# Optimization experiments

Hardware: AMD Instinct MI355X
Metric: run time of the kernel (lower is better)

Reference implementation:

```python
import jax, jax.numpy as jnp
import numpy as np

# dims
B_, L_, DIN, H, DOUT, NL = 2, 1024, 512, 768, 512, 4
ED, N, K = H, 16, 4            # expand_factor=1 -> d_inner=H; d_state=16; d_conv=4
DTR = (H + 15) // 16           # dt_rank = ceil(d_model/16) = 48


def setup_inputs() -> dict:
    key = jax.random.key(0)
    ks = iter(jax.random.split(key, 32))
    def g(shape, s=0.02):
        return jax.random.normal(next(ks), shape, jnp.float32) * s
    inp = dict(
        x=jax.random.normal(next(ks), (B_, L_, DIN), jnp.float32),
        in_proj_w=g((H, DIN)), in_proj_b=jnp.zeros((H,), jnp.float32),
        out_proj_w=g((DOUT, H)), out_proj_b=jnp.zeros((DOUT,), jnp.float32),
        ln1_w=jnp.ones((NL, H), jnp.float32), ln1_b=jnp.zeros((NL, H), jnp.float32),
        ln2_w=jnp.ones((NL, H), jnp.float32), ln2_b=jnp.zeros((NL, H), jnp.float32),
        ffn_w1=g((NL, 4 * H, H)), ffn_b1=jnp.zeros((NL, 4 * H), jnp.float32),
        ffn_w2=g((NL, H, 4 * H)), ffn_b2=jnp.zeros((NL, H), jnp.float32),
        rms_w=jnp.ones((NL, ED), jnp.float32),
        m_in_w=g((NL, 2 * ED, H)),
        conv_w=g((NL, ED, 1, K), 0.2), conv_b=jnp.zeros((NL, ED), jnp.float32),
        xproj_w=g((NL, DTR + 2 * N, ED)),
        dt_w=g((NL, ED, DTR), 0.1), dt_b=g((NL, ED), 0.1),
        A_log=jnp.log(jnp.tile(jnp.arange(1, N + 1, dtype=jnp.float32), (NL, ED, 1))),
        Dp=jnp.ones((NL, ED), jnp.float32),
        m_out_w=g((NL, H, ED)),
    )
    return inp


def _layernorm(x, w, b):
    m = x.mean(-1, keepdims=True)
    v = ((x - m) ** 2).mean(-1, keepdims=True)
    return (x - m) / jnp.sqrt(v + 1e-5) * w + b


def _rmsnorm(x, w):
    return x * jax.lax.rsqrt((x * x).mean(-1, keepdims=True) + 1e-5) * w


def _selective_scan(dA, dBx):
    # h_t = dA_t * h_{t-1} + dBx_t, done as a parallel associative scan over L
    def comb(c1, c2):
        a1, b1 = c1
        a2, b2 = c2
        return a1 * a2, a2 * b1 + b2
    _, h = jax.lax.associative_scan(comb, (dA, dBx), axis=1)
    return h  # (B, L, ED, N)


def _mamba(x, rw, iw, cw, cb, xw, dw, db, Alog, Dp, ow):
    # mambapy ResidualBlock: x + MambaBlock(RMSNorm(x))
    xn = _rmsnorm(x, rw)
    xz = xn @ iw.T                             # (B, L, 2*ED)
    xi, z = jnp.split(xz, 2, axis=-1)
    # causal depthwise conv1d (padding = K-1 left)
    xc = jax.lax.conv_general_dilated(
        xi.transpose(0, 2, 1), cw, (1,), [(K - 1, 0)],
        feature_group_count=ED, dimension_numbers=('NCH', 'OIH', 'NCH'))
    xi = jax.nn.silu(xc.transpose(0, 2, 1) + cb)
    dbc = xi @ xw.T                            # (B, L, DTR + 2N)
    d = dbc[..., :DTR]
    Bm = dbc[..., DTR:DTR + N]
    Cm = dbc[..., DTR + N:]
    delta = jax.nn.softplus(d @ dw.T + db)     # (B, L, ED)
    A = -jnp.exp(Alog)                         # (ED, N)
    dA = jnp.exp(delta[..., None] * A)         # (B, L, ED, N)
    dBx = (delta * xi)[..., None] * Bm[:, :, None, :]
    h = _selective_scan(dA, dBx)
    y = jnp.einsum('blen,bln->ble', h, Cm) + Dp * xi
    y = y * jax.nn.silu(z)
    return x + y @ ow.T


def reference(x, in_proj_w, in_proj_b, out_proj_w, out_proj_b,
              ln1_w, ln1_b, ln2_w, ln2_b,
              ffn_w1, ffn_b1, ffn_w2, ffn_b2,
              rms_w, m_in_w, conv_w, conv_b, xproj_w,
              dt_w, dt_b, A_log, Dp, m_out_w):
    h = x @ in_proj_w.T + in_proj_b
    for i in range(NL):
        h = h + _mamba(_layernorm(h, ln1_w[i], ln1_b[i]),
                       rms_w[i], m_in_w[i], conv_w[i], conv_b[i], xproj_w[i],
                       dt_w[i], dt_b[i], A_log[i], Dp[i], m_out_w[i])
        hn = _layernorm(h, ln2_w[i], ln2_b[i])
        h = h + jax.nn.relu(hn @ ffn_w1[i].T + ffn_b1[i]) @ ffn_w2[i].T + ffn_b2[i]
    return h @ out_proj_w.T + out_proj_b
```

## Files before the change

### kernel.cpp

```cpp
#include <hip/hip_runtime.h>
#include <stdint.h>

typedef unsigned short u16;
typedef __attribute__((ext_vector_type(8))) short short8;
typedef __attribute__((ext_vector_type(4))) float f32x4;

static __device__ __forceinline__ u16 f2bf(float f){
  unsigned int x = __float_as_uint(f);
  unsigned int r = (x + 0x7FFFu + ((x >> 16) & 1u)) >> 16;
  return (u16)r;
}
static __device__ __forceinline__ float bf2f(u16 u){
  return __uint_as_float(((unsigned int)u) << 16);
}

__global__ __launch_bounds__(256) void cvt_f32_bf16(const float* __restrict__ in,
                                                    u16* __restrict__ out, int n){
  int i = (blockIdx.x * 256 + threadIdx.x) * 4;
  int stride = gridDim.x * 256 * 4;
  for (; i < n; i += stride){
    float4 v = *reinterpret_cast<const float4*>(in + i);
    union { u16 u[4]; unsigned long long ll; } o;
    o.u[0] = f2bf(v.x); o.u[1] = f2bf(v.y); o.u[2] = f2bf(v.z); o.u[3] = f2bf(v.w);
    *reinterpret_cast<unsigned long long*>(out + i) = o.ll;
  }
}

__global__ __launch_bounds__(256) void build_dbc(const float* __restrict__ dt_w,
                                                 const float* __restrict__ xproj_w,
                                                 u16* __restrict__ out){
  const int total = 4 * 896 * 768;
  for (int idx = blockIdx.x * 256 + threadIdx.x; idx < total; idx += gridDim.x * 256){
    int l = idx / (896 * 768);
    int rem = idx - l * 896 * 768;
    int row = rem / 768;
    int k = rem - row * 768;
    float v = 0.f;
    if (row < 768){
      const float* dtr = dt_w + ((size_t)l * 768 + row) * 48;
      const float* xp  = xproj_w + (size_t)l * 80 * 768 + k;
      #pragma unroll 8
      for (int j = 0; j < 48; j++) v += dtr[j] * xp[(size_t)j * 768];
    } else if (row < 800){
      v = xproj_w[(size_t)l * 80 * 768 + (size_t)(48 + row - 768) * 768 + k];
    }
    out[idx] = f2bf(v);
  }
}

__global__ __launch_bounds__(256) void ln_rms_kernel(const float* __restrict__ in,
                                                     const float* __restrict__ w,
                                                     const float* __restrict__ b,
                                                     const float* __restrict__ rw,
                                                     float* __restrict__ xln,
                                                     u16* __restrict__ outB){
  int row = blockIdx.x;
  const float* x = in + (size_t)row * 768;
  int t = threadIdx.x;
  float v0 = x[t], v1 = x[t + 256], v2 = x[t + 512];
  float s = v0 + v1 + v2;
  float s2 = v0 * v0 + v1 * v1 + v2 * v2;
  #pragma unroll
  for (int off = 1; off < 64; off <<= 1){ s += __shfl_xor(s, off); s2 += __shfl_xor(s2, off); }
  __shared__ float red[8];
  int wid = t >> 6, lane = t & 63;
  if (lane == 0){ red[wid] = s; red[4 + wid] = s2; }
  __syncthreads();
  s = red[0] + red[1] + red[2] + red[3];
  s2 = red[4] + red[5] + red[6] + red[7];
  float mean = s * (1.f / 768.f);
  float var = s2 * (1.f / 768.f) - mean * mean;
  float rstd = rsqrtf(var + 1e-5f);
  float o0 = (v0 - mean) * rstd * w[t] + b[t];
  float o1 = (v1 - mean) * rstd * w[t + 256] + b[t + 256];
  float o2 = (v2 - mean) * rstd * w[t + 512] + b[t + 512];
  xln[(size_t)row * 768 + t]       = o0;
  xln[(size_t)row * 768 + t + 256] = o1;
  xln[(size_t)row * 768 + t + 512] = o2;
  float q = o0 * o0 + o1 * o1 + o2 * o2;
  #pragma unroll
  for (int off = 1; off < 64; off <<= 1){ q += __shfl_xor(q, off); }
  __syncthreads();
  if (lane == 0) red[wid] = q;
  __syncthreads();
  q = red[0] + red[1] + red[2] + red[3];
  float rs = rsqrtf(q * (1.f / 768.f) + 1e-5f);
  outB[(size_t)row * 768 + t]       = f2bf(o0 * rs * rw[t]);
  outB[(size_t)row * 768 + t + 256] = f2bf(o1 * rs * rw[t + 256]);
  outB[(size_t)row * 768 + t + 512] = f2bf(o2 * rs * rw[t + 512]);
}

__global__ __launch_bounds__(256) void ln_kernel(const float* __restrict__ in,
                                                 const float* __restrict__ w,
                                                 const float* __restrict__ b,
                                                 u16* __restrict__ outB){
  int row = blockIdx.x;
  const float* x = in + (size_t)row * 768;
  int t = threadIdx.x;
  float v0 = x[t], v1 = x[t + 256], v2 = x[t + 512];
  float s = v0 + v1 + v2;
  float s2 = v0 * v0 + v1 * v1 + v2 * v2;
  #pragma unroll
  for (int off = 1; off < 64; off <<= 1){ s += __shfl_xor(s, off); s2 += __shfl_xor(s2, off); }
  __shared__ float red[8];
  int wid = t >> 6, lane = t & 63;
  if (lane == 0){ red[wid] = s; red[4 + wid] = s2; }
  __syncthreads();
  s = red[0] + red[1] + red[2] + red[3];
  s2 = red[4] + red[5] + red[6] + red[7];
  float mean = s * (1.f / 768.f);
  float var = s2 * (1.f / 768.f) - mean * mean;
  float rstd = rsqrtf(var + 1e-5f);
  #pragma unroll
  for (int j = 0; j < 3; j++){
    int e = t + j * 256;
    float v = (j == 0) ? v0 : (j == 1) ? v1 : v2;
    outB[(size_t)row * 768 + e] = f2bf((v - mean) * rstd * w[e] + b[e]);
  }
}

__global__ __launch_bounds__(256) void conv_silu(const float* __restrict__ xz,
                                                 const float* __restrict__ cw,
                                                 const float* __restrict__ cb,
                                                 u16* __restrict__ xi){
  int row = blockIdx.x;
  int b = row >> 10, l = row & 1023;
  for (int e = threadIdx.x; e < 768; e += 256){
    const float* w = cw + (size_t)e * 4;
    float acc = cb[e];
    #pragma unroll
    for (int k = 0; k < 4; k++){
      int ls = l - 3 + k;
      if (ls >= 0) acc += w[k] * xz[((size_t)((b << 10) + ls)) * 1536 + e];
    }
    float sv = acc / (1.f + __expf(-acc));
    xi[(size_t)row * 768 + e] = f2bf(sv);
  }
}

__global__ __launch_bounds__(256) void scan_pass1(const float* __restrict__ delta,
                                                  const u16* __restrict__ xi,
                                                  const float* __restrict__ bc,
                                                  const float* __restrict__ A_log,
                                                  float* __restrict__ asum,
                                                  float* __restrict__ bsum){
  int bid = blockIdx.x;
  int eg = bid % 3; int c = (bid / 3) & 63; int b = bid / 192;
  int e = eg * 256 + threadIdx.x;
  float A[16], a[16], s[16];
  const float* al = A_log + (size_t)e * 16;
  #pragma unroll
  for (int n = 0; n < 16; n++){ A[n] = -__expf(al[n]); a[n] = 1.f; s[n] = 0.f; }
  for (int ll = 0; ll < 16; ll++){
    int row = b * 1024 + c * 16 + ll;
    float dlt = delta[(size_t)row * 768 + e];
    float xiv = bf2f(xi[(size_t)row * 768 + e]);
    float du = dlt * xiv;
    const float* bm = bc + (size_t)row * 32;
    #pragma unroll
    for (int n = 0; n < 16; n++){
      float dA = __expf(dlt * A[n]);
      s[n] = dA * s[n] + du * bm[n];
      a[n] *= dA;
    }
  }
  size_t base = (((size_t)(b * 64 + c) * 768) + e) * 16;
  #pragma unroll
  for (int n = 0; n < 16; n++){ asum[base + n] = a[n]; bsum[base + n] = s[n]; }
}

__global__ __launch_bounds__(256) void scan_pass2(const float* __restrict__ asum,
                                                  const float* __restrict__ bsum,
                                                  float* __restrict__ h0){
  int idx = blockIdx.x * 256 + threadIdx.x;
  int b = idx / 12288;
  int en = idx - b * 12288;
  float h = 0.f;
  for (int c = 0; c < 64; c++){
    size_t i = ((size_t)(b * 64 + c) * 12288) + en;
    h0[i] = h;
    h = asum[i] * h + bsum[i];
  }
}

__global__ __launch_bounds__(256) void scan_pass3(const float* __restrict__ delta,
                                                  const u16* __restrict__ xi,
                                                  const float* __restrict__ bc,
                                                  const float* __restrict__ A_log,
                                                  const float* __restrict__ h0,
                                                  const float* __restrict__ Dp,
                                                  const float* __restrict__ xz,
                                                  u16* __restrict__ y){
  int bid = blockIdx.x;
  int eg = bid % 3; int c = (bid / 3) & 63; int b = bid / 192;
  int e = eg * 256 + threadIdx.x;
  float A[16], s[16];
  const float* al = A_log + (size_t)e * 16;
  #pragma unroll
  for (int n = 0; n < 16; n++) A[n] = -__expf(al[n]);
  size_t base = (((size_t)(b * 64 + c) * 768) + e) * 16;
  #pragma unroll
  for (int n = 0; n < 16; n++) s[n] = h0[base + n];
  float dp = Dp[e];
  for (int ll = 0; ll < 16; ll++){
    int row = b * 1024 + c * 16 + ll;
    float dlt = delta[(size_t)row * 768 + e];
    float xiv = bf2f(xi[(size_t)row * 768 + e]);
    float du = dlt * xiv;
    const float* bm = bc + (size_t)row * 32;
    const float* cm = bm + 16;
    float acc = 0.f;
    #pragma unroll
    for (int n = 0; n < 16; n++){
      float dA = __expf(dlt * A[n]);
      s[n] = dA * s[n] + du * bm[n];
      acc += s[n] * cm[n];
    }
    float yv = acc + dp * xiv;
    float z = xz[(size_t)row * 1536 + 768 + e];
    yv *= z / (1.f + __expf(-z));
    y[(size_t)row * 768 + e] = f2bf(yv);
  }
}

template<int MODE>
__global__ __launch_bounds__(256) void gemm64(
    const u16* __restrict__ A, const u16* __restrict__ Bw, int N, int Kd,
    float* __restrict__ outF, u16* __restrict__ outB,
    const float* __restrict__ bias, const float* __restrict__ r1,
    const float* __restrict__ r2,
    float* __restrict__ dl, float* __restrict__ bco, const float* __restrict__ dtb){
  __shared__ u16 sm[4][2][64 * 64];
  const int tid = threadIdx.x;
  const int wid = tid >> 6, lane = tid & 63;
  const int lhi = lane >> 4, llo = lane & 15;
  int nwg = (int)(gridDim.x * gridDim.y);
  int orig = (int)(blockIdx.y * gridDim.x + blockIdx.x);
  int wg = (orig & 7) * (nwg >> 3) + (orig >> 3);
  int bx = wg & 31;
  int by = wg >> 5;
  const int m0 = bx * 64, n0 = by * 64;
  const int wm = (wid >> 1) * 32, wn = (wid & 1) * 32;
  const int nk = Kd >> 6;
  f32x4 acc[2][2] = {};

  auto stage = [&](int buf, int kt){
    const u16* Ab = A + (size_t)m0 * Kd + kt * 64;
    const u16* Bb = Bw + (size_t)n0 * Kd + kt * 64;
    #pragma unroll
    for (int j = 0; j < 2; j++){
      int sl = j * 256 + tid;
      int row = sl >> 3;
      int ch = (sl & 7) ^ (row & 7);
      __builtin_amdgcn_global_load_lds(
          (const __attribute__((address_space(1))) void*)(Ab + (size_t)row * Kd + ch * 8),
          (__attribute__((address_space(3))) void*)(&sm[buf][0][sl * 8]), 16, 0, 0);
    }
    #pragma unroll
    for (int j = 0; j < 2; j++){
      int sl = j * 256 + tid;
      int row = sl >> 3;
      int ch = (sl & 7) ^ (row & 7);
      __builtin_amdgcn_global_load_lds(
          (const __attribute__((address_space(1))) void*)(Bb + (size_t)row * Kd + ch * 8),
          (__attribute__((address_space(3))) void*)(&sm[buf][1][sl * 8]), 16, 0, 0);
    }
  };

  stage(0, 0);
  stage(1, 1);
  for (int kt = 0; kt < nk; ++kt){
    if (kt + 2 < nk){
      stage((kt + 2) & 3, kt + 2);
      asm volatile("s_waitcnt vmcnt(8)" ::: "memory");
    } else if (kt + 1 < nk){
      asm volatile("s_waitcnt vmcnt(4)" ::: "memory");
    } else {
      asm volatile("s_waitcnt vmcnt(0)" ::: "memory");
    }
    __builtin_amdgcn_s_barrier();
    __builtin_amdgcn_sched_barrier(0);
    const u16* Asb = &sm[kt & 3][0][0];
    const u16* Bsb = &sm[kt & 3][1][0];
    short8 af[2][2], bfr[2][2];
    #pragma unroll
    for (int mi = 0; mi < 2; mi++){
      int row = wm + mi * 16 + llo;
      const u16* rp = Asb + row * 64;
      #pragma unroll
      for (int s2 = 0; s2 < 2; s2++){
        int ch = (s2 * 4 + lhi) ^ (row & 7);
        af[mi][s2] = *(const short8*)(rp + ch * 8);
      }
    }
    #pragma unroll
    for (int ni = 0; ni < 2; ni++){
      int row = wn + ni * 16 + llo;
      const u16* rp = Bsb + row * 64;
      #pragma unroll
      for (int s2 = 0; s2 < 2; s2++){
        int ch = (s2 * 4 + lhi) ^ (row & 7);
        bfr[ni][s2] = *(const short8*)(rp + ch * 8);
      }
    }
    #pragma unroll
    for (int s2 = 0; s2 < 2; s2++)
      #pragma unroll
      for (int mi = 0; mi < 2; mi++)
        #pragma unroll
        for (int ni = 0; ni < 2; ni++)
          acc[mi][ni] = __builtin_amdgcn_mfma_f32_16x16x32_bf16(
              af[mi][s2], bfr[ni][s2], acc[mi][ni], 0, 0, 0);
  }
  #pragma unroll
  for (int mi = 0; mi < 2; mi++){
    #pragma unroll
    for (int ni = 0; ni < 2; ni++){
      int r0 = m0 + wm + mi * 16 + lhi * 4;
      int c = n0 + wn + ni * 16 + llo;
      #pragma unroll
      for (int r = 0; r < 4; r++){
        int rr = r0 + r;
        float v = acc[mi][ni][r];
        if (MODE == 0){
          size_t idx = (size_t)rr * N + c;
          if (bias) v += bias[c];
          if (r1) v += r1[idx];
          if (r2) v += r2[idx];
          outF[idx] = v;
          if (outB) outB[idx] = f2bf(v);
        } else if (MODE == 1){
          size_t idx = (size_t)rr * N + c;
          v += bias[c];
          outB[idx] = f2bf(v > 0.f ? v : 0.f);
        } else {
          if (c < 768){
            float tv = v + dtb[c];
            dl[(size_t)rr * 768 + c] = (tv > 20.f) ? tv : log1pf(__expf(tv));
          } else if (c < 800){
            bco[(size_t)rr * 32 + (c - 768)] = v;
          }
        }
      }
    }
  }
}

extern "C" void kernel_launch(void* const* d_in, const int* in_sizes, int n_in,
                              void* d_out, int out_size, void* d_ws, size_t ws_size,
                              hipStream_t stream){
  (void)in_sizes; (void)n_in; (void)out_size; (void)ws_size;
  const float* x_f       = (const float*)d_in[0];
  const float* in_proj_w = (const float*)d_in[1];
  const float* in_proj_b = (const float*)d_in[2];
  const float* out_proj_w= (const float*)d_in[3];
  const float* out_proj_b= (const float*)d_in[4];
  const float* ln1_w     = (const float*)d_in[5];
  const float* ln1_b     = (const float*)d_in[6];
  const float* ln2_w     = (const float*)d_in[7];
  const float* ln2_b     = (const float*)d_in[8];
  const float* ffn_w1    = (const float*)d_in[9];
  const float* ffn_b1    = (const float*)d_in[10];
  const float* ffn_w2    = (const float*)d_in[11];
  const float* ffn_b2    = (const float*)d_in[12];
  const float* rms_w     = (const float*)d_in[13];
  const float* m_in_w    = (const float*)d_in[14];
  const float* conv_w    = (const float*)d_in[15];
  const float* conv_b    = (const float*)d_in[16];
  const float* xproj_w   = (const float*)d_in[17];
  const float* dt_w      = (const float*)d_in[18];
  const float* dt_b      = (const float*)d_in[19];
  const float* A_log     = (const float*)d_in[20];
  const float* Dp        = (const float*)d_in[21];
  const float* m_out_w   = (const float*)d_in[22];

  char* ws = (char*)d_ws;
  size_t off = 0;
  auto alloc = [&](size_t bytes) -> char* {
    char* p = ws + off;
    off += (bytes + 255) & ~(size_t)255;
    return p;
  };
  u16* wb_inp  = (u16*)alloc((size_t)768 * 512 * 2);
  u16* wb_outp = (u16*)alloc((size_t)512 * 768 * 2);
  u16* wb_min  = (u16*)alloc((size_t)4 * 1536 * 768 * 2);
  u16* wb_mout = (u16*)alloc((size_t)4 * 768 * 768 * 2);
  u16* wb_f1   = (u16*)alloc((size_t)4 * 3072 * 768 * 2);
  u16* wb_f2   = (u16*)alloc((size_t)4 * 768 * 3072 * 2);
  u16* wb_dbc  = (u16*)alloc((size_t)4 * 896 * 768 * 2);
  u16* xbf     = (u16*)alloc((size_t)2048 * 512 * 2);
  float* hA    = (float*)alloc((size_t)2048 * 768 * 4);
  float* hB    = (float*)alloc((size_t)2048 * 768 * 4);
  float* xln   = (float*)alloc((size_t)2048 * 768 * 4);
  u16* xnbf    = (u16*)alloc((size_t)2048 * 768 * 2);
  float* xz    = (float*)alloc((size_t)2048 * 1536 * 4);
  u16* xibf    = (u16*)alloc((size_t)2048 * 768 * 2);
  float* dltb  = (float*)alloc((size_t)2048 * 768 * 4);
  float* bcb   = (float*)alloc((size_t)2048 * 32 * 4);
  float* asum  = (float*)alloc((size_t)2 * 64 * 768 * 16 * 4);
  float* bsum  = (float*)alloc((size_t)2 * 64 * 768 * 16 * 4);
  float* h0    = (float*)alloc((size_t)2 * 64 * 768 * 16 * 4);
  u16* ybf     = (u16*)alloc((size_t)2048 * 768 * 2);
  u16* tbf     = (u16*)alloc((size_t)2048 * 768 * 2);
  u16* f1bf    = (u16*)alloc((size_t)2048 * 3072 * 2);
  u16* hfbf    = (u16*)alloc((size_t)2048 * 768 * 2);

  auto cvt = [&](const float* in, u16* out, size_t n){
    int blocks = (int)((n / 4 + 255) / 256);
    if (blocks > 2048) blocks = 2048;
    cvt_f32_bf16<<<blocks, 256, 0, stream>>>(in, out, (int)n);
  };
  cvt(x_f, xbf, (size_t)2048 * 512);
  cvt(in_proj_w, wb_inp, (size_t)768 * 512);
  cvt(out_proj_w, wb_outp, (size_t)512 * 768);
  cvt(m_in_w, wb_min, (size_t)4 * 1536 * 768);
  cvt(m_out_w, wb_mout, (size_t)4 * 768 * 768);
  cvt(ffn_w1, wb_f1, (size_t)4 * 3072 * 768);
  cvt(ffn_w2, wb_f2, (size_t)4 * 768 * 3072);
  build_dbc<<<2048, 256, 0, stream>>>(dt_w, xproj_w, wb_dbc);

  auto gemm = [&](int mode, const u16* Ain, const u16* Bww, int N, int K,
                  float* oF, u16* oB, const float* bias, const float* rr1,
                  const float* rr2, float* dl, float* bco, const float* dtb){
    dim3 g(2048 / 64, N / 64), blk(256);
    if (mode == 0)
      gemm64<0><<<g, blk, 0, stream>>>(Ain, Bww, N, K, oF, oB, bias, rr1, rr2, dl, bco, dtb);
    else if (mode == 1)
      gemm64<1><<<g, blk, 0, stream>>>(Ain, Bww, N, K, oF, oB, bias, rr1, rr2, dl, bco, dtb);
    else
      gemm64<2><<<g, blk, 0, stream>>>(Ain, Bww, N, K, oF, oB, bias, rr1, rr2, dl, bco, dtb);
  };

  gemm(0, xbf, wb_inp, 768, 512, hA, nullptr, in_proj_b, nullptr, nullptr,
       nullptr, nullptr, nullptr);

  for (int i = 0; i < 4; i++){
    ln_rms_kernel<<<2048, 256, 0, stream>>>(hA, ln1_w + i * 768, ln1_b + i * 768,
                                            rms_w + i * 768, xln, xnbf);
    gemm(0, xnbf, wb_min + (size_t)i * 1536 * 768, 1536, 768, xz, nullptr,
         nullptr, nullptr, nullptr, nullptr, nullptr, nullptr);
    conv_silu<<<2048, 256, 0, stream>>>(xz, conv_w + (size_t)i * 768 * 4,
                                        conv_b + i * 768, xibf);
    gemm(2, xibf, wb_dbc + (size_t)i * 896 * 768, 896, 768, nullptr, nullptr,
         nullptr, nullptr, nullptr, dltb, bcb, dt_b + i * 768);
    scan_pass1<<<384, 256, 0, stream>>>(dltb, xibf, bcb,
                                        A_log + (size_t)i * 768 * 16, asum, bsum);
    scan_pass2<<<96, 256, 0, stream>>>(asum, bsum, h0);
    scan_pass3<<<384, 256, 0, stream>>>(dltb, xibf, bcb,
                                        A_log + (size_t)i * 768 * 16, h0,
                                        Dp + i * 768, xz, ybf);
    gemm(0, ybf, wb_mout + (size_t)i * 768 * 768, 768, 768, hB, nullptr,
         nullptr, hA, xln, nullptr, nullptr, nullptr);
    ln_kernel<<<2048, 256, 0, stream>>>(hB, ln2_w + i * 768, ln2_b + i * 768, tbf);
    gemm(1, tbf, wb_f1 + (size_t)i * 3072 * 768, 3072, 768, nullptr, f1bf,
         ffn_b1 + i * 3072, nullptr, nullptr, nullptr, nullptr, nullptr);
    gemm(0, f1bf, wb_f2 + (size_t)i * 768 * 3072, 768, 3072, hA,
         (i == 3) ? hfbf : nullptr, ffn_b2 + i * 768, hB, nullptr,
         nullptr, nullptr, nullptr);
  }
  gemm(0, hfbf, wb_outp, 512, 768, (float*)d_out, nullptr, out_proj_b,
       nullptr, nullptr, nullptr, nullptr, nullptr);
}
```

Baseline: 684.6 us.

## Enlarge GEMM tile to 128x64 with triple-buffered LDS and fuse weight conversions

The GEMM tile grows from 64x64 to 128x64. Each warp now computes 64x32, which raises arithmetic intensity and halves B-tile reloads across the M dimension. The LDS ring drops from 4 buffers to 3, and the next stage is issued after the barrier so the buffer it overwrites is safe to reuse. The seven separate f32-to-bf16 conversion launches become one launch with fixed segment offsets. Trade-offs: the grid halves, to 16 blocks by N/64, which lowers parallelism on a large-CU GPU, and a bigger register footprint under launch_bounds(256,2) may reduce occupancy.

```diff
diff --git a/kernel.cpp b/kernel.cpp
--- a/kernel.cpp
+++ b/kernel.cpp
@@ -14,16 +14,28 @@
   return __uint_as_float(((unsigned int)u) << 16);
 }
 
-__global__ __launch_bounds__(256) void cvt_f32_bf16(const float* __restrict__ in,
-                                                    u16* __restrict__ out, int n){
-  int i = (blockIdx.x * 256 + threadIdx.x) * 4;
-  int stride = gridDim.x * 256 * 4;
-  for (; i < n; i += stride){
-    float4 v = *reinterpret_cast<const float4*>(in + i);
-    union { u16 u[4]; unsigned long long ll; } o;
-    o.u[0] = f2bf(v.x); o.u[1] = f2bf(v.y); o.u[2] = f2bf(v.z); o.u[3] = f2bf(v.w);
-    *reinterpret_cast<unsigned long long*>(out + i) = o.ll;
-  }
+__global__ __launch_bounds__(256) void prep_cvt(
+    const float* __restrict__ s0, const float* __restrict__ s1,
+    const float* __restrict__ s2, const float* __restrict__ s3,
+    const float* __restrict__ s4, const float* __restrict__ s5,
+    const float* __restrict__ s6,
+    u16* __restrict__ d0, u16* __restrict__ d1, u16* __restrict__ d2,
+    u16* __restrict__ d3, u16* __restrict__ d4, u16* __restrict__ d5,
+    u16* __restrict__ d6){
+  size_t i = ((size_t)blockIdx.x * 256 + threadIdx.x) * 4;
+  const float* src; u16* dst; size_t base;
+  if      (i <  1048576){ src = s0; dst = d0; base = 0; }
+  else if (i <  1441792){ src = s1; dst = d1; base = 1048576; }
+  else if (i <  1835008){ src = s2; dst = d2; base = 1441792; }
+  else if (i <  6553600){ src = s3; dst = d3; base = 1835008; }
+  else if (i <  8912896){ src = s4; dst = d4; base = 6553600; }
+  else if (i < 18350080){ src = s5; dst = d5; base = 8912896; }
+  else                  { src = s6; dst = d6; base = 18350080; }
+  size_t o = i - base;
+  float4 v = *reinterpret_cast<const float4*>(src + o);
+  union { u16 u[4]; unsigned long long ll; } t;
+  t.u[0] = f2bf(v.x); t.u[1] = f2bf(v.y); t.u[2] = f2bf(v.z); t.u[3] = f2bf(v.w);
+  *reinterpret_cast<unsigned long long*>(dst + o) = t.ll;
 }
 
 __global__ __launch_bounds__(256) void build_dbc(const float* __restrict__ dt_w,
@@ -224,37 +236,36 @@
 }
 
 template<int MODE>
-__global__ __launch_bounds__(256) void gemm64(
+__global__ __launch_bounds__(256, 2) void gemm128x64(
     const u16* __restrict__ A, const u16* __restrict__ Bw, int N, int Kd,
     float* __restrict__ outF, u16* __restrict__ outB,
     const float* __restrict__ bias, const float* __restrict__ r1,
     const float* __restrict__ r2,
     float* __restrict__ dl, float* __restrict__ bco, const float* __restrict__ dtb){
-  __shared__ u16 sm[4][2][64 * 64];
+  __shared__ u16 sm[3][(128 + 64) * 64];
   const int tid = threadIdx.x;
   const int wid = tid >> 6, lane = tid & 63;
   const int lhi = lane >> 4, llo = lane & 15;
+  const int wr = wid >> 1, wc = wid & 1;
   int nwg = (int)(gridDim.x * gridDim.y);
   int orig = (int)(blockIdx.y * gridDim.x + blockIdx.x);
   int wg = (orig & 7) * (nwg >> 3) + (orig >> 3);
-  int bx = wg & 31;
-  int by = wg >> 5;
-  const int m0 = bx * 64, n0 = by * 64;
-  const int wm = (wid >> 1) * 32, wn = (wid & 1) * 32;
+  const int m0 = (wg & 15) * 128, n0 = (wg >> 4) * 64;
   const int nk = Kd >> 6;
-  f32x4 acc[2][2] = {};
+  f32x4 acc[4][2] = {};
 
   auto stage = [&](int buf, int kt){
     const u16* Ab = A + (size_t)m0 * Kd + kt * 64;
     const u16* Bb = Bw + (size_t)n0 * Kd + kt * 64;
-    #pragma unroll
-    for (int j = 0; j < 2; j++){
+    u16* base = &sm[buf][0];
+    #pragma unroll
+    for (int j = 0; j < 4; j++){
       int sl = j * 256 + tid;
       int row = sl >> 3;
       int ch = (sl & 7) ^ (row & 7);
       __builtin_amdgcn_global_load_lds(
           (const __attribute__((address_space(1))) void*)(Ab + (size_t)row * Kd + ch * 8),
-          (__attribute__((address_space(3))) void*)(&sm[buf][0][sl * 8]), 16, 0, 0);
+          (__attribute__((address_space(3))) void*)(base + sl * 8), 16, 0, 0);
     }
     #pragma unroll
     for (int j = 0; j < 2; j++){
@@ -263,29 +274,32 @@
       int ch = (sl & 7) ^ (row & 7);
       __builtin_amdgcn_global_load_lds(
           (const __attribute__((address_space(1))) void*)(Bb + (size_t)row * Kd + ch * 8),
-          (__attribute__((address_space(3))) void*)(&sm[buf][1][sl * 8]), 16, 0, 0);
+          (__attribute__((address_space(3))) void*)(base + 128 * 64 + sl * 8), 16, 0, 0);
     }
   };
 
   stage(0, 0);
-  stage(1, 1);
+  if (nk > 1) stage(1, 1);
+  int bsel = 2;
   for (int kt = 0; kt < nk; ++kt){
-    if (kt + 2 < nk){
-      stage((kt + 2) & 3, kt + 2);
-      asm volatile("s_waitcnt vmcnt(8)" ::: "memory");
-    } else if (kt + 1 < nk){
-      asm volatile("s_waitcnt vmcnt(4)" ::: "memory");
+    if (kt + 1 < nk){
+      asm volatile("s_waitcnt vmcnt(6)" ::: "memory");
     } else {
       asm volatile("s_waitcnt vmcnt(0)" ::: "memory");
     }
     __builtin_amdgcn_s_barrier();
     __builtin_amdgcn_sched_barrier(0);
-    const u16* Asb = &sm[kt & 3][0][0];
-    const u16* Bsb = &sm[kt & 3][1][0];
-    short8 af[2][2], bfr[2][2];
-    #pragma unroll
-    for (int mi = 0; mi < 2; mi++){
-      int row = wm + mi * 16 + llo;
+    if (kt + 2 < nk){
+      stage(bsel, kt + 2);
+      bsel = (bsel == 2) ? 0 : bsel + 1;
+    }
+    int cb = kt % 3;
+    const u16* Asb = &sm[cb][0];
+    const u16* Bsb = &sm[cb][128 * 64];
+    short8 af[4][2], bfr[2][2];
+    #pragma unroll
+    for (int mi = 0; mi < 4; mi++){
+      int row = wr * 64 + mi * 16 + llo;
       const u16* rp = Asb + row * 64;
       #pragma unroll
       for (int s2 = 0; s2 < 2; s2++){
@@ -295,7 +309,7 @@
     }
     #pragma unroll
     for (int ni = 0; ni < 2; ni++){
-      int row = wn + ni * 16 + llo;
+      int row = wc * 32 + ni * 16 + llo;
       const u16* rp = Bsb + row * 64;
       #pragma unroll
       for (int s2 = 0; s2 < 2; s2++){
@@ -306,18 +320,18 @@
     #pragma unroll
     for (int s2 = 0; s2 < 2; s2++)
       #pragma unroll
-      for (int mi = 0; mi < 2; mi++)
+      for (int mi = 0; mi < 4; mi++)
         #pragma unroll
         for (int ni = 0; ni < 2; ni++)
           acc[mi][ni] = __builtin_amdgcn_mfma_f32_16x16x32_bf16(
               af[mi][s2], bfr[ni][s2], acc[mi][ni], 0, 0, 0);
   }
   #pragma unroll
-  for (int mi = 0; mi < 2; mi++){
+  for (int mi = 0; mi < 4; mi++){
     #pragma unroll
     for (int ni = 0; ni < 2; ni++){
-      int r0 = m0 + wm + mi * 16 + lhi * 4;
-      int c = n0 + wn + ni * 16 + llo;
+      int r0 = m0 + wr * 64 + mi * 16 + lhi * 4;
+      int c = n0 + wc * 32 + ni * 16 + llo;
       #pragma unroll
       for (int r = 0; r < 4; r++){
         int rr = r0 + r;
@@ -405,30 +419,22 @@
   u16* f1bf    = (u16*)alloc((size_t)2048 * 3072 * 2);
   u16* hfbf    = (u16*)alloc((size_t)2048 * 768 * 2);
 
-  auto cvt = [&](const float* in, u16* out, size_t n){
-    int blocks = (int)((n / 4 + 255) / 256);
-    if (blocks > 2048) blocks = 2048;
-    cvt_f32_bf16<<<blocks, 256, 0, stream>>>(in, out, (int)n);
-  };
-  cvt(x_f, xbf, (size_t)2048 * 512);
-  cvt(in_proj_w, wb_inp, (size_t)768 * 512);
-  cvt(out_proj_w, wb_outp, (size_t)512 * 768);
-  cvt(m_in_w, wb_min, (size_t)4 * 1536 * 768);
-  cvt(m_out_w, wb_mout, (size_t)4 * 768 * 768);
-  cvt(ffn_w1, wb_f1, (size_t)4 * 3072 * 768);
-  cvt(ffn_w2, wb_f2, (size_t)4 * 768 * 3072);
+  prep_cvt<<<27136, 256, 0, stream>>>(x_f, in_proj_w, out_proj_w, m_in_w,
+                                      m_out_w, ffn_w1, ffn_w2,
+                                      xbf, wb_inp, wb_outp, wb_min,
+                                      wb_mout, wb_f1, wb_f2);
   build_dbc<<<2048, 256, 0, stream>>>(dt_w, xproj_w, wb_dbc);
 
   auto gemm = [&](int mode, const u16* Ain, const u16* Bww, int N, int K,
                   float* oF, u16* oB, const float* bias, const float* rr1,
                   const float* rr2, float* dl, float* bco, const float* dtb){
-    dim3 g(2048 / 64, N / 64), blk(256);
+    dim3 g(16, N / 64), blk(256);
     if (mode == 0)
-      gemm64<0><<<g, blk, 0, stream>>>(Ain, Bww, N, K, oF, oB, bias, rr1, rr2, dl, bco, dtb);
+      gemm128x64<0><<<g, blk, 0, stream>>>(Ain, Bww, N, K, oF, oB, bias, rr1, rr2, dl, bco, dtb);
     else if (mode == 1)
-      gemm64<1><<<g, blk, 0, stream>>>(Ain, Bww, N, K, oF, oB, bias, rr1, rr2, dl, bco, dtb);
+      gemm128x64<1><<<g, blk, 0, stream>>>(Ain, Bww, N, K, oF, oB, bias, rr1, rr2, dl, bco, dtb);
     else
-      gemm64<2><<<g, blk, 0, stream>>>(Ain, Bww, N, K, oF, oB, bias, rr1, rr2, dl, bco, dtb);
+      gemm128x64<2><<<g, blk, 0, stream>>>(Ain, Bww, N, K, oF, oB, bias, rr1, rr2, dl, bco, dtb);
   };
 
   gemm(0, xbf, wb_inp, 768, 512, hA, nullptr, in_proj_b, nullptr, nullptr,
```

Measured after the change: 725.9 us. +6.0%, slower.
